# Optimization experiments

Measured on AMD Instinct MI355X. Metric: run time of the kernel, lower is better.

## Reference

```python
import jax, jax.numpy as jnp
import numpy as np

B, N, C_IN, C_MID, H, N_CLS = 128, 2048, 3, 64, 128, 40
EPS = 1e-5

def setup_inputs() -> dict:
    key = jax.random.key(0)
    ks = jax.random.split(key, 12)
    sc = lambda fan: 1.0 / np.sqrt(fan)
    return {
        "x": jax.random.normal(ks[0], (B, N, C_IN), jnp.float32),
        "conv_w": jax.random.normal(ks[1], (C_MID, C_IN), jnp.float32) * sc(C_IN),
        "conv_b": jnp.zeros((C_MID,), jnp.float32),
        "gamma": jnp.ones((C_MID,), jnp.float32),
        "beta": jnp.zeros((C_MID,), jnp.float32),
        "running_mean": jax.random.normal(ks[2], (C_MID,), jnp.float32) * 0.1,
        "running_var": jax.random.uniform(ks[3], (C_MID,), jnp.float32) + 0.5,
        "W_ih": jax.random.normal(ks[4], (4 * H, C_MID), jnp.float32) * sc(H),
        "W_hh": jax.random.normal(ks[5], (4 * H, H), jnp.float32) * sc(H),
        "b_ih": jax.random.normal(ks[6], (4 * H,), jnp.float32) * sc(H),
        "b_hh": jax.random.normal(ks[7], (4 * H,), jnp.float32) * sc(H),
        "W_out": jax.random.normal(ks[8], (N_CLS, H), jnp.float32) * sc(H),
        "b_out": jnp.zeros((N_CLS,), jnp.float32),
    }

def reference(x, conv_w, conv_b, gamma, beta, running_mean, running_var,
              W_ih, W_hh, b_ih, b_hh, W_out, b_out):
    # Conv1d(3,64,1) == per-point linear; BN (inference form) + ReLU.  [B,N,64]
    h = jnp.einsum('bnc,oc->bno', x, conv_w) + conv_b
    inv = gamma * jax.lax.rsqrt(running_var + EPS)
    h = jax.nn.relu((h - running_mean) * inv + beta)
    # Precompute input-side gate projections for all timesteps: [B,N,4H]
    xg = jnp.einsum('bnc,gc->bng', h, W_ih) + b_ih + b_hh
    Whh_T = W_hh.T  # [H,4H]

    def step(carry, xg_t):
        h_prev, c_prev = carry
        g = xg_t + h_prev @ Whh_T  # [B,4H]
        i, f, gg, o = jnp.split(g, 4, axis=-1)  # PyTorch gate order i,f,g,o
        i = jax.nn.sigmoid(i)
        f = jax.nn.sigmoid(f)
        gg = jnp.tanh(gg)
        o = jax.nn.sigmoid(o)
        c = f * c_prev + i * gg
        h_new = o * jnp.tanh(c)
        return (h_new, c), None

    init = (jnp.zeros((x.shape[0], W_hh.shape[1]), x.dtype),
            jnp.zeros((x.shape[0], W_hh.shape[1]), x.dtype))
    (h_last, _), _ = jax.lax.scan(step, init, jnp.swapaxes(xg, 0, 1))
    # Only the last timestep feeds the classifier head.
    return h_last @ W_out.T + b_out
```

## Files before the change

### kernel.cpp

```cpp
#include <hip/hip_runtime.h>
#include <math.h>

#define BB 128
#define NN 2048
#define CIN 3
#define CMID 64
#define HH 128
#define G4 512
#define NCLS 40
#define EPSV 1e-5f

__device__ __forceinline__ float fsigmoid(float x) {
    return 1.0f / (1.0f + __expf(-x));
}
__device__ __forceinline__ float ftanh(float x) {
    return 2.0f / (1.0f + __expf(-2.0f * x)) - 1.0f;
}

__global__ __launch_bounds__(512, 2)
void lstm_seq_kernel(const float* __restrict__ x,
                     const float* __restrict__ conv_w, const float* __restrict__ conv_b,
                     const float* __restrict__ gamma,  const float* __restrict__ beta,
                     const float* __restrict__ rmean,  const float* __restrict__ rvar,
                     const float* __restrict__ W_ih,   const float* __restrict__ W_hh,
                     const float* __restrict__ b_ih,   const float* __restrict__ b_hh,
                     const float* __restrict__ W_out,  const float* __restrict__ b_out,
                     float* __restrict__ out)
{
    __shared__ float x_s[NN * CIN];
    __shared__ float hc_s[CMID];
    __shared__ float h_s[HH];
    __shared__ float g_s[G4];

    const int b = blockIdx.x;
    const int t = threadIdx.x;

    const float* xb = x + (size_t)b * NN * CIN;
    for (int i = t; i < NN * CIN; i += 512) x_s[i] = xb[i];

    float ca0 = 0.f, ca1 = 0.f, ca2 = 0.f, cd = 0.f;
    if (t < CMID) {
        float inv = gamma[t] * rsqrtf(rvar[t] + EPSV);
        ca0 = conv_w[t * 3 + 0] * inv;
        ca1 = conv_w[t * 3 + 1] * inv;
        ca2 = conv_w[t * 3 + 2] * inv;
        cd  = (conv_b[t] - rmean[t]) * inv + beta[t];
    }
    if (t < HH) h_s[t] = 0.0f;

    float4 wih[CMID / 4];
    {
        const float4* p = (const float4*)(W_ih + (size_t)t * CMID);
        #pragma unroll
        for (int i = 0; i < CMID / 4; ++i) wih[i] = p[i];
    }
    float4 whh[HH / 4];
    {
        const float4* p = (const float4*)(W_hh + (size_t)t * HH);
        #pragma unroll
        for (int i = 0; i < HH / 4; ++i) whh[i] = p[i];
    }
    const float bias = b_ih[t] + b_hh[t];
    const bool is_tanh_gate = (t >= 2 * HH) && (t < 3 * HH);

    float c_reg = 0.0f;

    __syncthreads();

    for (int n = 0; n < NN; ++n) {
        if (t < CMID) {
            float xv0 = x_s[n * 3 + 0];
            float xv1 = x_s[n * 3 + 1];
            float xv2 = x_s[n * 3 + 2];
            float hc = cd + ca0 * xv0 + ca1 * xv1 + ca2 * xv2;
            hc_s[t] = fmaxf(hc, 0.0f);
        }
        __syncthreads();

        float g0 = bias, g1 = 0.f, g2 = 0.f, g3 = 0.f;
        const float4* hc4 = (const float4*)hc_s;
        #pragma unroll
        for (int c = 0; c < CMID / 4; ++c) {
            float4 v = hc4[c];
            float4 w = wih[c];
            g0 += w.x * v.x; g1 += w.y * v.y; g2 += w.z * v.z; g3 += w.w * v.w;
        }
        const float4* h4 = (const float4*)h_s;
        #pragma unroll
        for (int k = 0; k < HH / 4; ++k) {
            float4 v = h4[k];
            float4 w = whh[k];
            g0 += w.x * v.x; g1 += w.y * v.y; g2 += w.z * v.z; g3 += w.w * v.w;
        }
        float g = (g0 + g1) + (g2 + g3);

        float act = is_tanh_gate ? ftanh(g) : fsigmoid(g);
        g_s[t] = act;
        __syncthreads();

        if (t < HH) {
            float iv = g_s[t];
            float fv = g_s[HH + t];
            float gv = g_s[2 * HH + t];
            float ov = g_s[3 * HH + t];
            c_reg = fv * c_reg + iv * gv;
            h_s[t] = ov * ftanh(c_reg);
        }
        __syncthreads();
    }

    if (t < NCLS) {
        float acc = b_out[t];
        const float* wrow = W_out + (size_t)t * HH;
        #pragma unroll
        for (int j = 0; j < HH; ++j) acc += wrow[j] * h_s[j];
        out[(size_t)b * NCLS + t] = acc;
    }
}

extern "C" void kernel_launch(void* const* d_in, const int* in_sizes, int n_in,
                              void* d_out, int out_size, void* d_ws, size_t ws_size,
                              hipStream_t stream) {
    const float* x      = (const float*)d_in[0];
    const float* conv_w = (const float*)d_in[1];
    const float* conv_b = (const float*)d_in[2];
    const float* gamma  = (const float*)d_in[3];
    const float* beta   = (const float*)d_in[4];
    const float* rmean  = (const float*)d_in[5];
    const float* rvar   = (const float*)d_in[6];
    const float* W_ih   = (const float*)d_in[7];
    const float* W_hh   = (const float*)d_in[8];
    const float* b_ih   = (const float*)d_in[9];
    const float* b_hh   = (const float*)d_in[10];
    const float* W_out  = (const float*)d_in[11];
    const float* b_out  = (const float*)d_in[12];
    float* out = (float*)d_out;

    lstm_seq_kernel<<<BB, 512, 0, stream>>>(x, conv_w, conv_b, gamma, beta,
                                            rmean, rvar, W_ih, W_hh, b_ih, b_hh,
                                            W_out, b_out, out);
}
```

Measured before the change: 2.409 ms.

## Split LSTM gate dot products across 8-lane groups with shuffle reduction

```diff
diff --git a/kernel.cpp b/kernel.cpp
--- a/kernel.cpp
+++ b/kernel.cpp
@@ -3,21 +3,26 @@
 
 #define BB 128
 #define NN 2048
-#define CIN 3
 #define CMID 64
 #define HH 128
-#define G4 512
 #define NCLS 40
+#define CHUNK 128
 #define EPSV 1e-5f
 
 __device__ __forceinline__ float fsigmoid(float x) {
     return 1.0f / (1.0f + __expf(-x));
 }
-__device__ __forceinline__ float ftanh(float x) {
+__device__ __forceinline__ float ftanh2(float x) {
     return 2.0f / (1.0f + __expf(-2.0f * x)) - 1.0f;
 }
+__device__ __forceinline__ void fma4(float& a, const float4 w, const float4 v) {
+    a = fmaf(w.x, v.x, a);
+    a = fmaf(w.y, v.y, a);
+    a = fmaf(w.z, v.z, a);
+    a = fmaf(w.w, v.w, a);
+}
 
-__global__ __launch_bounds__(512, 2)
+__global__ __launch_bounds__(1024, 4)
 void lstm_seq_kernel(const float* __restrict__ x,
                      const float* __restrict__ conv_w, const float* __restrict__ conv_b,
                      const float* __restrict__ gamma,  const float* __restrict__ beta,
@@ -27,93 +32,106 @@
                      const float* __restrict__ W_out,  const float* __restrict__ b_out,
                      float* __restrict__ out)
 {
-    __shared__ float x_s[NN * CIN];
-    __shared__ float hc_s[CMID];
-    __shared__ float h_s[HH];
-    __shared__ float g_s[G4];
+    __shared__ float hc_s[CHUNK][CMID];
+    __shared__ float h_p[2][8][20];
+    __shared__ float cA0[CMID], cA1[CMID], cA2[CMID], cD[CMID];
 
+    const int t = threadIdx.x;
     const int b = blockIdx.x;
-    const int t = threadIdx.x;
+    const int j = t >> 3;
+    const int s = t & 7;
 
-    const float* xb = x + (size_t)b * NN * CIN;
-    for (int i = t; i < NN * CIN; i += 512) x_s[i] = xb[i];
-
-    float ca0 = 0.f, ca1 = 0.f, ca2 = 0.f, cd = 0.f;
     if (t < CMID) {
         float inv = gamma[t] * rsqrtf(rvar[t] + EPSV);
-        ca0 = conv_w[t * 3 + 0] * inv;
-        ca1 = conv_w[t * 3 + 1] * inv;
-        ca2 = conv_w[t * 3 + 2] * inv;
-        cd  = (conv_b[t] - rmean[t]) * inv + beta[t];
+        cA0[t] = conv_w[t * 3 + 0] * inv;
+        cA1[t] = conv_w[t * 3 + 1] * inv;
+        cA2[t] = conv_w[t * 3 + 2] * inv;
+        cD[t]  = (conv_b[t] - rmean[t]) * inv + beta[t];
     }
-    if (t < HH) h_s[t] = 0.0f;
+    if (t < 2 * 8 * 20) ((float*)h_p)[t] = 0.0f;
 
-    float4 wih[CMID / 4];
-    {
-        const float4* p = (const float4*)(W_ih + (size_t)t * CMID);
+    float4 wih[4][2];
+    float4 whh[4][4];
+    float bias[4];
+    #pragma unroll
+    for (int g = 0; g < 4; ++g) {
+        const int r = g * HH + j;
+        const float* pih = W_ih + (size_t)r * CMID + s * 8;
+        wih[g][0] = *(const float4*)(pih);
+        wih[g][1] = *(const float4*)(pih + 4);
+        const float* phh = W_hh + (size_t)r * HH + s * 16;
         #pragma unroll
-        for (int i = 0; i < CMID / 4; ++i) wih[i] = p[i];
+        for (int i2 = 0; i2 < 4; ++i2) whh[g][i2] = *(const float4*)(phh + 4 * i2);
+        bias[g] = b_ih[r] + b_hh[r];
     }
-    float4 whh[HH / 4];
-    {
-        const float4* p = (const float4*)(W_hh + (size_t)t * HH);
-        #pragma unroll
-        for (int i = 0; i < HH / 4; ++i) whh[i] = p[i];
-    }
-    const float bias = b_ih[t] + b_hh[t];
-    const bool is_tanh_gate = (t >= 2 * HH) && (t < 3 * HH);
 
     float c_reg = 0.0f;
+    const float* xb = x + (size_t)b * NN * 3;
 
-    __syncthreads();
+    for (int ch = 0; ch < NN / CHUNK; ++ch) {
+        const int base = ch * CHUNK;
+        __syncthreads();
 
-    for (int n = 0; n < NN; ++n) {
-        if (t < CMID) {
-            float xv0 = x_s[n * 3 + 0];
-            float xv1 = x_s[n * 3 + 1];
-            float xv2 = x_s[n * 3 + 2];
-            float hc = cd + ca0 * xv0 + ca1 * xv1 + ca2 * xv2;
-            hc_s[t] = fmaxf(hc, 0.0f);
+        #pragma unroll
+        for (int i = 0; i < (CHUNK * CMID) / 1024; ++i) {
+            int v  = i * 1024 + t;
+            int n  = v >> 6;
+            int cc = v & 63;
+            float x0 = xb[(base + n) * 3 + 0];
+            float x1 = xb[(base + n) * 3 + 1];
+            float x2 = xb[(base + n) * 3 + 2];
+            float hcv = cD[cc] + cA0[cc] * x0 + cA1[cc] * x1 + cA2[cc] * x2;
+            hc_s[n][cc] = fmaxf(hcv, 0.0f);
         }
         __syncthreads();
 
-        float g0 = bias, g1 = 0.f, g2 = 0.f, g3 = 0.f;
-        const float4* hc4 = (const float4*)hc_s;
-        #pragma unroll
-        for (int c = 0; c < CMID / 4; ++c) {
-            float4 v = hc4[c];
-            float4 w = wih[c];
-            g0 += w.x * v.x; g1 += w.y * v.y; g2 += w.z * v.z; g3 += w.w * v.w;
+        for (int k = 0; k < CHUNK; ++k) {
+            const int p = (base + k) & 1;
+            float a0 = 0.f, a1 = 0.f, a2 = 0.f, a3 = 0.f;
+
+            const float4* hcp = (const float4*)(&hc_s[k][s * 8]);
+            const float4* hp4 = (const float4*)(&h_p[p][s][0]);
+
+            float4 v0 = hcp[0];
+            float4 v1 = hcp[1];
+            fma4(a0, wih[0][0], v0); fma4(a1, wih[1][0], v0);
+            fma4(a2, wih[2][0], v0); fma4(a3, wih[3][0], v0);
+            fma4(a0, wih[0][1], v1); fma4(a1, wih[1][1], v1);
+            fma4(a2, wih[2][1], v1); fma4(a3, wih[3][1], v1);
+
+            #pragma unroll
+            for (int i2 = 0; i2 < 4; ++i2) {
+                float4 u = hp4[i2];
+                fma4(a0, whh[0][i2], u); fma4(a1, whh[1][i2], u);
+                fma4(a2, whh[2][i2], u); fma4(a3, whh[3][i2], u);
+            }
+
+            #pragma unroll
+            for (int m = 1; m <= 4; m <<= 1) {
+                a0 += __shfl_xor(a0, m);
+                a1 += __shfl_xor(a1, m);
+                a2 += __shfl_xor(a2, m);
+                a3 += __shfl_xor(a3, m);
+            }
+
+            float gi = fsigmoid(a0 + bias[0]);
+            float gf = fsigmoid(a1 + bias[1]);
+            float gg = ftanh2(a2 + bias[2]);
+            float go = fsigmoid(a3 + bias[3]);
+            c_reg = gf * c_reg + gi * gg;
+            float hv = go * ftanh2(c_reg);
+
+            if (s == 0) h_p[p ^ 1][j >> 4][j & 15] = hv;
+            __syncthreads();
         }
-        const float4* h4 = (const float4*)h_s;
-        #pragma unroll
-        for (int k = 0; k < HH / 4; ++k) {
-            float4 v = h4[k];
-            float4 w = whh[k];
-            g0 += w.x * v.x; g1 += w.y * v.y; g2 += w.z * v.z; g3 += w.w * v.w;
-        }
-        float g = (g0 + g1) + (g2 + g3);
-
-        float act = is_tanh_gate ? ftanh(g) : fsigmoid(g);
-        g_s[t] = act;
-        __syncthreads();
-
-        if (t < HH) {
-            float iv = g_s[t];
-            float fv = g_s[HH + t];
-            float gv = g_s[2 * HH + t];
-            float ov = g_s[3 * HH + t];
-            c_reg = fv * c_reg + iv * gv;
-            h_s[t] = ov * ftanh(c_reg);
-        }
-        __syncthreads();
     }
 
     if (t < NCLS) {
         float acc = b_out[t];
-        const float* wrow = W_out + (size_t)t * HH;
+        const float* wr = W_out + (size_t)t * HH;
         #pragma unroll
-        for (int j = 0; j < HH; ++j) acc += wrow[j] * h_s[j];
+        for (int jj = 0; jj < HH; ++jj)
+            acc = fmaf(wr[jj], h_p[0][jj >> 4][jj & 15], acc);
         out[(size_t)b * NCLS + t] = acc;
     }
 }
@@ -136,7 +154,7 @@
     const float* b_out  = (const float*)d_in[12];
     float* out = (float*)d_out;
 
-    lstm_seq_kernel<<<BB, 512, 0, stream>>>(x, conv_w, conv_b, gamma, beta,
-                                            rmean, rvar, W_ih, W_hh, b_ih, b_hh,
-                                            W_out, b_out, out);
+    lstm_seq_kernel<<<BB, 1024, 0, stream>>>(x, conv_w, conv_b, gamma, beta,
+                                             rmean, rvar, W_ih, W_hh, b_ih, b_hh,
+                                             W_out, b_out, out);
 }
```

Measured after the change: 2.535 ms. +5.2%, slower.
